# Kernel tuning notes

Measured on AMD Instinct MI355X. Metric: run time of the kernel, lower is better.

## Reference

```python
import jax, jax.numpy as jnp
import numpy as np

VOCAB, EMB, HID, OUT = 32000, 512, 1024, 8
B, S = 128, 512


def setup_inputs() -> dict:
    key = jax.random.key(0)
    ks = jax.random.split(key, 7)
    sequence_ids = jax.random.randint(ks[0], (B, S), 0, VOCAB)
    scale = 0.02
    emb = jax.random.normal(ks[1], (VOCAB, EMB), dtype=jnp.float32) * scale
    W_ih = jax.random.normal(ks[2], (4 * HID, EMB), dtype=jnp.float32) * scale
    W_hh = jax.random.normal(ks[3], (4 * HID, HID), dtype=jnp.float32) * scale
    b = jax.random.normal(ks[4], (4 * HID,), dtype=jnp.float32) * scale
    W_out = jax.random.normal(ks[5], (OUT, HID), dtype=jnp.float32) * scale
    b_out = jax.random.normal(ks[6], (OUT,), dtype=jnp.float32) * scale
    return {"sequence_ids": sequence_ids, "emb": emb, "W_ih": W_ih, "W_hh": W_hh,
            "b": b, "W_out": W_out, "b_out": b_out}


def reference(sequence_ids, emb, W_ih, W_hh, b, W_out, b_out):
    # embedding lookup: [B, S, E]
    x = emb[sequence_ids]
    Bb = x.shape[0]
    H = W_hh.shape[1]
    # precompute input projections for all timesteps at once: [S, B, 4H]
    xg = jnp.einsum('bse,ge->sbg', x, W_ih) + b

    def step(carry, xg_t):
        h, c = carry
        gates = xg_t + h @ W_hh.T  # [B, 4H]
        i, f, g, o = jnp.split(gates, 4, axis=-1)
        c = jax.nn.sigmoid(f) * c + jax.nn.sigmoid(i) * jnp.tanh(g)
        h = jax.nn.sigmoid(o) * jnp.tanh(c)
        return (h, c), None

    h0 = jnp.zeros((Bb, H), x.dtype)
    (h_last, _), _ = jax.lax.scan(step, (h0, h0), xg)
    # classifier on last hidden state: [B, OUT]
    return h_last @ W_out.T + b_out
```

## Files before the change

### kernel.cpp

```cpp
#include <hip/hip_runtime.h>
#include <cstdint>
#include <cstddef>

#define SEQ    512
#define BATCH  128
#define EMB    512
#define HID    1024
#define KTOT   1536
#define NOUT   8

#define RG     4
#define NBQ    64
#define NBLK   (RG*NBQ)
#define ROWS   32

typedef unsigned short u16;
typedef unsigned int   u32;
typedef unsigned long long u64;
typedef __attribute__((ext_vector_type(8))) __bf16 bf16x8;
typedef __attribute__((ext_vector_type(4))) float  f32x4;
typedef __attribute__((ext_vector_type(4))) float  float4v;
typedef __attribute__((ext_vector_type(4))) u16    u16x4;

#define OFF_X    0ull
#define SZ_X     ((size_t)SEQ*BATCH*EMB*2)
#define OFF_W    (OFF_X + SZ_X)
#define SZ_W     ((size_t)4*HID*KTOT*2)
#define OFF_RING (OFF_W + SZ_W)
#define SZ_RING  ((size_t)(SEQ+1)*BATCH*HID*2)
#define OFF_FW   (OFF_RING + SZ_RING)
#define SZ_FW    ((size_t)RG*NBQ*4*64)
#define WS_NEED  (OFF_FW + SZ_FW)

__device__ inline u16 f2b(float f) {
  uint32_t u = __builtin_bit_cast(uint32_t, f);
  u = u + 0x7FFFu + ((u >> 16) & 1u);
  return (u16)(u >> 16);
}
__device__ inline float b2f(u16 u) {
  uint32_t v = ((uint32_t)u) << 16;
  return __builtin_bit_cast(float, v);
}
__device__ inline float sigm(float x) { return 1.0f / (1.0f + __expf(-x)); }
__device__ inline float tanh_(float x) {
  x = fminf(fmaxf(x, -15.f), 15.f);
  float e = __expf(2.f * x);
  return (e - 1.f) / (e + 1.f);
}
__device__ inline f32x4 mfma16(bf16x8 a, bf16x8 b, f32x4 c) {
  return __builtin_amdgcn_mfma_f32_16x16x32_bf16(a, b, c, 0, 0, 0);
}

__global__ void embed_kernel(const int* __restrict__ ids,
                             const float* __restrict__ emb,
                             u16* __restrict__ x) {
  int bid = blockIdx.x;
  int t = bid >> 7, b = bid & 127;
  int idx = ids[b * SEQ + t];
  const float4v* src = (const float4v*)(emb + (size_t)idx * EMB);
  float4v v = src[threadIdx.x];
  u16x4 o;
  o.x = f2b(v.x); o.y = f2b(v.y); o.z = f2b(v.z); o.w = f2b(v.w);
  *(u16x4*)(x + (size_t)bid * EMB + threadIdx.x * 4) = o;
}

__global__ void wpack_kernel(const float* __restrict__ Wih,
                             const float* __restrict__ Whh,
                             u16* __restrict__ Wp) {
  int gc = blockIdx.x;
  int unit = gc >> 2, q = gc & 3;
  int row = q * HID + unit;
  u16* dst = Wp + (size_t)gc * KTOT;
  for (int k = threadIdx.x; k < KTOT; k += 256) {
    float v = (k < EMB) ? Wih[(size_t)row * EMB + k]
                        : Whh[(size_t)row * HID + (k - EMB)];
    dst[k] = f2b(v);
  }
}

__global__ __launch_bounds__(256, 1) void lstm_kernel(
    const u16* __restrict__ x,
    const u16* __restrict__ Wp,
    const float* __restrict__ bias,
    u16* __restrict__ ring,
    u32* __restrict__ fw)
{
  __shared__ float pacc[4][ROWS][68];

  const int tid  = threadIdx.x;
  const int bid  = blockIdx.x;
  const int rg   = bid & 3;
  const int nb   = bid >> 2;
  const int lane = tid & 63;
  const int kq   = tid >> 6;
  const int l15  = lane & 15;
  const int lhi  = lane >> 4;

  const int nxc  = (kq == 0) ? 12 : (kq == 1 ? 4 : 0);
  const int arow = rg * ROWS + l15;

  u32* fw_own = &fw[(((size_t)rg * NBQ + nb) * 4 + kq) * 16];
  const int pbase = (kq == 1) ? 0 : (kq == 2 ? 16 : 40);
  const int nflag = (kq == 1) ? 64 : 96;
  const u32* fp0 = &fw[(((size_t)rg * NBQ + pbase + (lane >> 2)) * 4 + (lane & 3)) * 16];
  const int  f2i = lane + 64;
  const u32* fp1 = (f2i < nflag)
      ? &fw[(((size_t)rg * NBQ + pbase + (f2i >> 2)) * 4 + (f2i & 3)) * 16]
      : fp0;

  bf16x8 wreg[12][4];
  {
    const int colbase = nb * 64;
    #pragma unroll
    for (int c = 0; c < 12; ++c)
      #pragma unroll
      for (int nt = 0; nt < 4; ++nt)
        wreg[c][nt] = *(const bf16x8*)(Wp
            + (size_t)(colbase + nt * 16 + l15) * KTOT
            + kq * 384 + c * 32 + lhi * 8);
  }

  const int urow = tid >> 3;
  const int up   = tid & 7;
  const int rowg = rg * ROWS + urow;
  float bs[2][4];
  #pragma unroll
  for (int k = 0; k < 2; ++k) {
    int ug = nb * 16 + 2 * up + k;
    #pragma unroll
    for (int q = 0; q < 4; ++q) bs[k][q] = bias[q * HID + ug];
  }
  float cst[2] = {0.f, 0.f};

  bf16x8 af[2][12];
  #pragma unroll
  for (int c = 0; c < 12; ++c)
    if (c < nxc) {
      #pragma unroll
      for (int mt = 0; mt < 2; ++mt)
        af[mt][c] = *(const bf16x8*)(x + (size_t)(arow + mt * 16) * EMB
                                     + kq * 384 + c * 32 + lhi * 8);
    }

  #pragma unroll 1
  for (int t = 0; t < SEQ; ++t) {
    f32x4 acc[2][4];
    #pragma unroll
    for (int mt = 0; mt < 2; ++mt)
      #pragma unroll
      for (int nt = 0; nt < 4; ++nt) acc[mt][nt] = (f32x4){0.f, 0.f, 0.f, 0.f};
    #pragma unroll
    for (int c = 0; c < 12; ++c)
      if (c < nxc) {
        #pragma unroll
        for (int mt = 0; mt < 2; ++mt)
          #pragma unroll
          for (int nt = 0; nt < 4; ++nt)
            acc[mt][nt] = mfma16(af[mt][c], wreg[c][nt], acc[mt][nt]);
      }

    if (t > 0 && kq > 0) {
      const u32 tgt = (u32)t;
      int bail = 0;
      for (;;) {
        u32 a = __hip_atomic_load(fp0, __ATOMIC_RELAXED, __HIP_MEMORY_SCOPE_AGENT);
        u32 b = __hip_atomic_load(fp1, __ATOMIC_RELAXED, __HIP_MEMORY_SCOPE_AGENT);
        if (__all((a >= tgt) & (b >= tgt))) break;
        if (++bail > (1 << 20)) break;
        __builtin_amdgcn_s_sleep(1);
      }
      __asm__ __volatile__("" ::: "memory");
    }

    {
      const u16* hb = ring + (size_t)t * (BATCH * HID);
      #pragma unroll
      for (int c = 0; c < 12; ++c)
        if (c >= nxc) {
          #pragma unroll
          for (int mt = 0; mt < 2; ++mt)
            af[mt][c] = *(const bf16x8*)(hb + (size_t)(arow + mt * 16) * HID
                                         + (kq * 384 - 512 + c * 32) + lhi * 8);
        }
    }

    {
      int tn = (t + 1 < SEQ) ? (t + 1) : t;
      const u16* xb = x + (size_t)tn * (BATCH * EMB);
      #pragma unroll
      for (int c = 0; c < 12; ++c)
        if (c < nxc) {
          #pragma unroll
          for (int mt = 0; mt < 2; ++mt)
            af[mt][c] = *(const bf16x8*)(xb + (size_t)(arow + mt * 16) * EMB
                                         + kq * 384 + c * 32 + lhi * 8);
        }
    }

    #pragma unroll
    for (int c = 0; c < 12; ++c)
      if (c >= nxc) {
        #pragma unroll
        for (int mt = 0; mt < 2; ++mt)
          #pragma unroll
          for (int nt = 0; nt < 4; ++nt)
            acc[mt][nt] = mfma16(af[mt][c], wreg[c][nt], acc[mt][nt]);
      }

    #pragma unroll
    for (int mt = 0; mt < 2; ++mt)
      #pragma unroll
      for (int nt = 0; nt < 4; ++nt)
        #pragma unroll
        for (int rr = 0; rr < 4; ++rr) {
          int row = mt * 16 + lhi * 4 + rr;
          int c   = nt * 16 + l15;
          int pc  = (c & ~7) | ((c ^ row) & 7);
          pacc[kq][row][pc] = acc[mt][nt][rr];
        }
    __syncthreads();

    float s[2][4];
    #pragma unroll
    for (int k = 0; k < 2; ++k)
      #pragma unroll
      for (int q = 0; q < 4; ++q) s[k][q] = bs[k][q];
    #pragma unroll
    for (int k2 = 0; k2 < 4; ++k2)
      #pragma unroll
      for (int cl = 0; cl < 8; ++cl) {
        int pc = 8 * up + ((cl ^ urow) & 7);
        s[cl >> 2][cl & 3] += pacc[k2][urow][pc];
      }
    __syncthreads();

    {
      float hv2[2];
      #pragma unroll
      for (int k = 0; k < 2; ++k) {
        float cn = sigm(s[k][1]) * cst[k] + sigm(s[k][0]) * tanh_(s[k][2]);
        cst[k] = cn;
        hv2[k] = sigm(s[k][3]) * tanh_(cn);
      }
      u32 val = (u32)f2b(hv2[0]) | ((u32)f2b(hv2[1]) << 16);
      u32* dst = (u32*)(ring + (size_t)(t + 1) * (BATCH * HID)
                        + (size_t)rowg * HID + nb * 16 + 2 * up);
      asm volatile("global_store_dword %0, %1, off sc0 sc1"
                   :: "v"(dst), "v"(val) : "memory");
    }
    asm volatile("s_waitcnt vmcnt(0)" ::: "memory");

    if (t < SEQ - 1 && lane == 0) {
      __hip_atomic_store(fw_own, (u32)(t + 1), __ATOMIC_RELAXED,
                         __HIP_MEMORY_SCOPE_AGENT);
    }
  }
}

__global__ void head_kernel(const u16* __restrict__ h,
                            const float* __restrict__ Wout,
                            const float* __restrict__ bout,
                            float* __restrict__ out) {
  int b = blockIdx.x, l = threadIdx.x;
  float p[NOUT];
  #pragma unroll
  for (int o = 0; o < NOUT; ++o) p[o] = 0.f;
  for (int k = l; k < HID; k += 64) {
    float hv = b2f(h[(size_t)b * HID + k]);
    #pragma unroll
    for (int o = 0; o < NOUT; ++o) p[o] += hv * Wout[(size_t)o * HID + k];
  }
  #pragma unroll
  for (int o = 0; o < NOUT; ++o) {
    float v = p[o];
    #pragma unroll
    for (int off = 32; off > 0; off >>= 1) v += __shfl_down(v, off);
    if (l == 0) out[b * NOUT + o] = v + bout[o];
  }
}

__global__ void sentinel_kernel(float* out, int n) {
  int i = blockIdx.x * 256 + threadIdx.x;
  if (i < n) out[i] = 1e9f;
}

extern "C" void kernel_launch(void* const* d_in, const int* in_sizes, int n_in,
                              void* d_out, int out_size, void* d_ws, size_t ws_size,
                              hipStream_t stream) {
  const int*   ids  = (const int*)d_in[0];
  const float* emb  = (const float*)d_in[1];
  const float* Wih  = (const float*)d_in[2];
  const float* Whh  = (const float*)d_in[3];
  const float* bias = (const float*)d_in[4];
  const float* Wout = (const float*)d_in[5];
  const float* bout = (const float*)d_in[6];
  float* out = (float*)d_out;

  if (ws_size < WS_NEED) {
    sentinel_kernel<<<(out_size + 255) / 256, 256, 0, stream>>>(out, out_size);
    return;
  }

  char* ws = (char*)d_ws;
  u16* x    = (u16*)(ws + OFF_X);
  u16* Wp   = (u16*)(ws + OFF_W);
  u16* ring = (u16*)(ws + OFF_RING);
  u32* fwv  = (u32*)(ws + OFF_FW);

  hipMemsetAsync(ring, 0, (size_t)BATCH * HID * 2, stream);
  hipMemsetAsync(fwv, 0, SZ_FW, stream);

  embed_kernel<<<SEQ * BATCH, 128, 0, stream>>>(ids, emb, x);
  wpack_kernel<<<4 * HID, 256, 0, stream>>>(Wih, Whh, Wp);

  lstm_kernel<<<NBLK, 256, 0, stream>>>(x, Wp, bias, ring, fwv);

  head_kernel<<<BATCH, 64, 0, stream>>>(ring + (size_t)SEQ * BATCH * HID,
                                        Wout, bout, out);
}
```

Measured before the change: 3.073 ms.

## Replace per-step flag handshake with sentinel-filled ring polling on hidden state

Drops the per-block progress flags and the flag spin-wait. The whole hidden-state ring is pre-filled with an all-ones sentinel, and consumer waves load h_t directly, re-polling with cache-bypassing loads until no sentinel words remain. This removes the flag store, the store-drain wait and the separate flag polling from the critical path of each timestep, and lets the h load be issued before the x-part MFMAs. In exchange it adds a full ring fill pass (~130MB of writes) before the recurrence. It also relies on each 16-byte load seeing an h write atomically and on no real bf16 pair ever equalling the sentinel, and it shrinks the bailout limit.

```diff
diff --git a/kernel.cpp b/kernel.cpp
--- a/kernel.cpp
+++ b/kernel.cpp
@@ -13,14 +13,15 @@
 #define NBQ    64
 #define NBLK   (RG*NBQ)
 #define ROWS   32
+#define SENT   0xFFFFFFFFu
 
 typedef unsigned short u16;
 typedef unsigned int   u32;
-typedef unsigned long long u64;
 typedef __attribute__((ext_vector_type(8))) __bf16 bf16x8;
 typedef __attribute__((ext_vector_type(4))) float  f32x4;
 typedef __attribute__((ext_vector_type(4))) float  float4v;
 typedef __attribute__((ext_vector_type(4))) u16    u16x4;
+typedef __attribute__((ext_vector_type(4))) u32    u32x4;
 
 #define OFF_X    0ull
 #define SZ_X     ((size_t)SEQ*BATCH*EMB*2)
@@ -28,9 +29,7 @@
 #define SZ_W     ((size_t)4*HID*KTOT*2)
 #define OFF_RING (OFF_W + SZ_W)
 #define SZ_RING  ((size_t)(SEQ+1)*BATCH*HID*2)
-#define OFF_FW   (OFF_RING + SZ_RING)
-#define SZ_FW    ((size_t)RG*NBQ*4*64)
-#define WS_NEED  (OFF_FW + SZ_FW)
+#define WS_NEED  (OFF_RING + SZ_RING)
 
 __device__ inline u16 f2b(float f) {
   uint32_t u = __builtin_bit_cast(uint32_t, f);
@@ -49,6 +48,16 @@
 }
 __device__ inline f32x4 mfma16(bf16x8 a, bf16x8 b, f32x4 c) {
   return __builtin_amdgcn_mfma_f32_16x16x32_bf16(a, b, c, 0, 0, 0);
+}
+
+__global__ void fill_kernel(u32* __restrict__ p, size_t n4) {
+  size_t i = (size_t)blockIdx.x * 256 + threadIdx.x;
+  u32x4 s = (u32x4){SENT, SENT, SENT, SENT};
+  for (; i < n4; i += (size_t)gridDim.x * 256) {
+    u32* dst = p + i * 4;
+    asm volatile("global_store_dwordx4 %0, %1, off sc0 sc1 nt"
+                 :: "v"(dst), "v"(s) : "memory");
+  }
 }
 
 __global__ void embed_kernel(const int* __restrict__ ids,
@@ -82,8 +91,7 @@
     const u16* __restrict__ x,
     const u16* __restrict__ Wp,
     const float* __restrict__ bias,
-    u16* __restrict__ ring,
-    u32* __restrict__ fw)
+    u16* __restrict__ ring)
 {
   __shared__ float pacc[4][ROWS][68];
 
@@ -99,15 +107,6 @@
   const int nxc  = (kq == 0) ? 12 : (kq == 1 ? 4 : 0);
   const int arow = rg * ROWS + l15;
 
-  u32* fw_own = &fw[(((size_t)rg * NBQ + nb) * 4 + kq) * 16];
-  const int pbase = (kq == 1) ? 0 : (kq == 2 ? 16 : 40);
-  const int nflag = (kq == 1) ? 64 : 96;
-  const u32* fp0 = &fw[(((size_t)rg * NBQ + pbase + (lane >> 2)) * 4 + (lane & 3)) * 16];
-  const int  f2i = lane + 64;
-  const u32* fp1 = (f2i < nflag)
-      ? &fw[(((size_t)rg * NBQ + pbase + (f2i >> 2)) * 4 + (f2i & 3)) * 16]
-      : fp0;
-
   bf16x8 wreg[12][4];
   {
     const int colbase = nb * 64;
@@ -144,6 +143,17 @@
 
   #pragma unroll 1
   for (int t = 0; t < SEQ; ++t) {
+    const u16* hb = ring + (size_t)t * (BATCH * HID);
+
+    #pragma unroll
+    for (int c = 0; c < 12; ++c)
+      if (c >= nxc) {
+        #pragma unroll
+        for (int mt = 0; mt < 2; ++mt)
+          af[mt][c] = *(const bf16x8*)(hb + (size_t)(arow + mt * 16) * HID
+                                       + (kq * 384 - 512 + c * 32) + lhi * 8);
+      }
+
     f32x4 acc[2][4];
     #pragma unroll
     for (int mt = 0; mt < 2; ++mt)
@@ -158,31 +168,6 @@
           for (int nt = 0; nt < 4; ++nt)
             acc[mt][nt] = mfma16(af[mt][c], wreg[c][nt], acc[mt][nt]);
       }
-
-    if (t > 0 && kq > 0) {
-      const u32 tgt = (u32)t;
-      int bail = 0;
-      for (;;) {
-        u32 a = __hip_atomic_load(fp0, __ATOMIC_RELAXED, __HIP_MEMORY_SCOPE_AGENT);
-        u32 b = __hip_atomic_load(fp1, __ATOMIC_RELAXED, __HIP_MEMORY_SCOPE_AGENT);
-        if (__all((a >= tgt) & (b >= tgt))) break;
-        if (++bail > (1 << 20)) break;
-        __builtin_amdgcn_s_sleep(1);
-      }
-      __asm__ __volatile__("" ::: "memory");
-    }
-
-    {
-      const u16* hb = ring + (size_t)t * (BATCH * HID);
-      #pragma unroll
-      for (int c = 0; c < 12; ++c)
-        if (c >= nxc) {
-          #pragma unroll
-          for (int mt = 0; mt < 2; ++mt)
-            af[mt][c] = *(const bf16x8*)(hb + (size_t)(arow + mt * 16) * HID
-                                         + (kq * 384 - 512 + c * 32) + lhi * 8);
-        }
-    }
 
     {
       int tn = (t + 1 < SEQ) ? (t + 1) : t;
@@ -197,6 +182,39 @@
         }
     }
 
+    if (kq > 0) {
+      int bail = 0;
+      for (;;) {
+        bool ok = true;
+        #pragma unroll
+        for (int c = 0; c < 12; ++c)
+          if (c >= nxc) {
+            #pragma unroll
+            for (int mt = 0; mt < 2; ++mt) {
+              u32x4 v = __builtin_bit_cast(u32x4, af[mt][c]);
+              ok = ok & (v.x != SENT) & (v.y != SENT)
+                      & (v.z != SENT) & (v.w != SENT);
+            }
+          }
+        if (__all(ok)) break;
+        if (++bail > (1 << 16)) break;
+        __builtin_amdgcn_s_sleep(1);
+        #pragma unroll
+        for (int c = 0; c < 12; ++c)
+          if (c >= nxc) {
+            #pragma unroll
+            for (int mt = 0; mt < 2; ++mt) {
+              const u16* p = hb + (size_t)(arow + mt * 16) * HID
+                             + (kq * 384 - 512 + c * 32) + lhi * 8;
+              asm volatile("global_load_dwordx4 %0, %1, off sc0 sc1"
+                           : "=&v"(af[mt][c]) : "v"(p) : "memory");
+            }
+          }
+        asm volatile("s_waitcnt vmcnt(0)" ::: "memory");
+        __builtin_amdgcn_sched_barrier(0);
+      }
+    }
+
     #pragma unroll
     for (int c = 0; c < 12; ++c)
       if (c >= nxc) {
@@ -247,12 +265,6 @@
                         + (size_t)rowg * HID + nb * 16 + 2 * up);
       asm volatile("global_store_dword %0, %1, off sc0 sc1"
                    :: "v"(dst), "v"(val) : "memory");
-    }
-    asm volatile("s_waitcnt vmcnt(0)" ::: "memory");
-
-    if (t < SEQ - 1 && lane == 0) {
-      __hip_atomic_store(fw_own, (u32)(t + 1), __ATOMIC_RELAXED,
-                         __HIP_MEMORY_SCOPE_AGENT);
     }
   }
 }
@@ -305,15 +317,17 @@
   u16* x    = (u16*)(ws + OFF_X);
   u16* Wp   = (u16*)(ws + OFF_W);
   u16* ring = (u16*)(ws + OFF_RING);
-  u32* fwv  = (u32*)(ws + OFF_FW);
 
   hipMemsetAsync(ring, 0, (size_t)BATCH * HID * 2, stream);
-  hipMemsetAsync(fwv, 0, SZ_FW, stream);
+  {
+    size_t n4 = (size_t)SEQ * BATCH * HID * 2 / 16;
+    fill_kernel<<<2048, 256, 0, stream>>>((u32*)(ring + (size_t)BATCH * HID), n4);
+  }
 
   embed_kernel<<<SEQ * BATCH, 128, 0, stream>>>(ids, emb, x);
   wpack_kernel<<<4 * HID, 256, 0, stream>>>(Wih, Whh, Wp);
 
-  lstm_kernel<<<NBLK, 256, 0, stream>>>(x, Wp, bias, ring, fwv);
+  lstm_kernel<<<NBLK, 256, 0, stream>>>(x, Wp, bias, ring);
 
   head_kernel<<<BATCH, 64, 0, stream>>>(ring + (size_t)SEQ * BATCH * HID,
                                         Wout, bout, out);
```

New measurement: 4.898 ms. 1.59x slower.
